# Optimization experiments

Measured on AMD Instinct MI355X. Metric: run time of the kernel, lower is better.

## Reference

```python
import jax, jax.numpy as jnp
import numpy as np

DIM_IN, DIM_Q, DIM_K, DIM_S, DIM_MLP_S, L, B = 512, 128, 128, 256, 128, 512, 32


def setup_inputs() -> dict:
    key = jax.random.key(0)
    ks = jax.random.split(key, 16)
    s = lambda fan_in: 1.0 / np.sqrt(fan_in)
    inp = {
        "query": jax.random.normal(ks[0], (B, L, DIM_IN), jnp.float32),
        "key": jax.random.normal(ks[1], (B, L, DIM_IN), jnp.float32),
        "value": jax.random.normal(ks[2], (B, L, DIM_IN), jnp.float32),
        "sf": jax.random.normal(ks[3], (B, DIM_S), jnp.float32),
        "atten_mask": jax.random.randint(ks[4], (B, L, L), 0, 2).astype(bool),
        # linear weights stored (in, out); y = x @ W + b
        "Wq": jax.random.normal(ks[5], (DIM_IN, DIM_Q), jnp.float32) * s(DIM_IN),
        "bq": jnp.zeros((DIM_Q,), jnp.float32),
        "Wk": jax.random.normal(ks[6], (DIM_IN, DIM_K), jnp.float32) * s(DIM_IN),
        "bk": jnp.zeros((DIM_K,), jnp.float32),
        "Wv": jax.random.normal(ks[7], (DIM_IN, DIM_K), jnp.float32) * s(DIM_IN),
        "bv": jnp.zeros((DIM_K,), jnp.float32),
        "Wb1": jax.random.normal(ks[8], (DIM_S, DIM_MLP_S), jnp.float32) * s(DIM_S),
        "bb1": jnp.zeros((DIM_MLP_S,), jnp.float32),
        "Wb2": jax.random.normal(ks[9], (DIM_MLP_S, L * L), jnp.float32) * s(DIM_MLP_S),
        "bb2": jnp.zeros((L * L,), jnp.float32),
    }
    return inp


def reference(query, key, value, sf, atten_mask, Wq, bq, Wk, bk, Wv, bv, Wb1, bb1, Wb2, bb2):
    b, l, d = query.shape
    q = query @ Wq + bq          # [b, l, dim_q]
    k = key @ Wk + bk            # [b, l, dim_k]
    v = value @ Wv + bv          # [b, l, dim_k]
    # bias MLP: Linear -> ReLU -> Linear, reshaped to [b, l, l]
    bias = (jax.nn.relu(sf @ Wb1 + bb1) @ Wb2 + bb2).reshape(b, l, l)
    scale = q.shape[-1] ** 0.5
    scores = jnp.einsum("bld,bmd->blm", q, k) / scale
    # faithful to masked_fill_(mask, 1e-9): masked positions become 1e-9, NOT -inf
    scores = jnp.where(atten_mask, jnp.asarray(1e-9, scores.dtype), scores)
    attn = jax.nn.softmax(scores, axis=-1) + bias   # bias added AFTER softmax
    out = jnp.einsum("blm,bmd->bld", attn, v)
    return out
```

## Files before the change

### kernel.cpp

```cpp
#include <hip/hip_runtime.h>


typedef unsigned int   u32;
typedef unsigned short u16;
typedef __attribute__((ext_vector_type(8))) short bf16x8;
typedef __attribute__((ext_vector_type(4))) float f32x4;
typedef __attribute__((ext_vector_type(4))) u32   u32x4;

__device__ __forceinline__ float B2F(u16 x) { return __uint_as_float(((u32)x) << 16); }
__device__ __forceinline__ u16 f2bf(float f) {
    u32 u = __float_as_uint(f);
    return (u16)((u + 0x7fffu + ((u >> 16) & 1u)) >> 16);
}

__global__ __launch_bounds__(256) void prep(
    const void* __restrict__ mask, u32* __restrict__ flag, int detN,
    const float* __restrict__ Wq, const float* __restrict__ Wk, const float* __restrict__ Wv,
    u16* __restrict__ WT,
    const float* __restrict__ sf, const float* __restrict__ Wb1,
    const float* __restrict__ bb1, float* __restrict__ hT)
{
    __shared__ u16 Ts[64][136];
    const int blk = blockIdx.x, tid = threadIdx.x;

    if (blk < detN) {
        const u32* m = (const u32*)mask;
        const size_t t = (size_t)blk * 256 + tid;
        u32 any = 0;
#pragma unroll
        for (int l = 0; l < 4; ++l) any |= (m[t * 4 + l] > 1u) ? 1u : 0u;
        if (__ballot(any)) {
            if ((tid & 63) == 0) atomicOr(flag, 1u);
        }
        return;
    }
    if (blk < detN + 24) {
        const int widx = blk - detN;
        const int s = widx >> 3, kt = widx & 7;
        const float* W = (s == 0) ? Wq : (s == 1) ? Wk : Wv;
        {
            const int kk = tid >> 2, nseg = tid & 3;
            const float4* src = (const float4*)(W + (size_t)(kt * 64 + kk) * 128 + nseg * 32);
#pragma unroll
            for (int j = 0; j < 8; ++j) {
                float4 v = src[j];
                Ts[kk][nseg * 32 + j * 4 + 0] = f2bf(v.x);
                Ts[kk][nseg * 32 + j * 4 + 1] = f2bf(v.y);
                Ts[kk][nseg * 32 + j * 4 + 2] = f2bf(v.z);
                Ts[kk][nseg * 32 + j * 4 + 3] = f2bf(v.w);
            }
        }
        __syncthreads();
        {
            const int n = tid >> 1, kseg = tid & 1;
            u32 pk[16];
#pragma unroll
            for (int j = 0; j < 16; ++j)
                pk[j] = (u32)Ts[kseg * 32 + 2 * j][n] | ((u32)Ts[kseg * 32 + 2 * j + 1][n] << 16);
            u32x4* dst = (u32x4*)(WT + (size_t)s * 65536 + (size_t)n * 512 + kt * 64 + kseg * 32);
            dst[0] = (u32x4){pk[0], pk[1], pk[2], pk[3]};
            dst[1] = (u32x4){pk[4], pk[5], pk[6], pk[7]};
            dst[2] = (u32x4){pk[8], pk[9], pk[10], pk[11]};
            dst[3] = (u32x4){pk[12], pk[13], pk[14], pk[15]};
        }
        return;
    }
    {
        const int t = (blk - detN - 24) * 256 + tid;
        const int b = t >> 7, n = t & 127;
        float acc = bb1[n];
        for (int m = 0; m < 256; ++m)
            acc += sf[b * 256 + m] * Wb1[m * 128 + n];
        hT[n * 32 + b] = fmaxf(acc, 0.0f);
    }
}

__global__ __launch_bounds__(256) void mid(
    const float* __restrict__ Xq, const float* __restrict__ Xk, const float* __restrict__ Xv,
    const u16* __restrict__ WT,
    const float* __restrict__ Bq, const float* __restrict__ Bk, const float* __restrict__ Bv,
    u16* __restrict__ Yq, u16* __restrict__ Yk, u16* __restrict__ YvT,
    const float* __restrict__ hT, const float* __restrict__ Wb2,
    const float* __restrict__ bb2, u16* __restrict__ biasb,
    const void* __restrict__ mask, const u32* __restrict__ flag, int mode,
    unsigned char* __restrict__ canonbuf)
{
    __shared__ u16 Xs[64][72];
    __shared__ u16 Ws[128][72];
    const int blk = blockIdx.x, tid = threadIdx.x;

    if (blk < 512) {
        const size_t n0 = ((size_t)blk * 256 + tid) * 2;
        float ax[32], ay[32];
        {
            const float2 bb = *(const float2*)&bb2[n0];
#pragma unroll
            for (int b = 0; b < 32; ++b) { ax[b] = bb.x; ay[b] = bb.y; }
        }
#pragma unroll 2
        for (int m = 0; m < 128; ++m) {
            const float2 w2 = *(const float2*)&Wb2[(size_t)m * 262144 + n0];
            const float* hrow = hT + m * 32;
#pragma unroll
            for (int b = 0; b < 32; ++b) {
                const float hv = hrow[b];
                ax[b] += w2.x * hv;
                ay[b] += w2.y * hv;
            }
        }
#pragma unroll
        for (int b = 0; b < 32; ++b) {
            const u32 pk = (u32)f2bf(ax[b]) | ((u32)f2bf(ay[b]) << 16);
            *(u32*)(biasb + (size_t)b * 262144 + n0) = pk;
        }
        return;
    }

    if (blk < 1280) {
        const int pidx = blk - 512;
        const int s = pidx >> 8;
        const int R0 = (pidx & 255) * 64;
        const float* X; const float* Bi;
        if (s == 0)      { X = Xq; Bi = Bq; }
        else if (s == 1) { X = Xk; Bi = Bk; }
        else             { X = Xv; Bi = Bv; }
        const u16* Wn = WT + (size_t)s * 65536;

        const int w    = tid >> 6;
        const int lane = tid & 63;
        const int c    = lane & 15;
        const int qd   = lane >> 4;

        f32x4 acc[8];
#pragma unroll
        for (int t = 0; t < 8; ++t) acc[t] = (f32x4){0.f, 0.f, 0.f, 0.f};

        for (int kc = 0; kc < 8; ++kc) {
            __syncthreads();
            {
                const int row = tid >> 2, seg = tid & 3;
                const float4* src = (const float4*)(X + (size_t)(R0 + row) * 512 + kc * 64 + seg * 16);
                float4 v0 = src[0], v1 = src[1], v2 = src[2], v3 = src[3];
                u32 pk[8];
                pk[0] = (u32)f2bf(v0.x) | ((u32)f2bf(v0.y) << 16);
                pk[1] = (u32)f2bf(v0.z) | ((u32)f2bf(v0.w) << 16);
                pk[2] = (u32)f2bf(v1.x) | ((u32)f2bf(v1.y) << 16);
                pk[3] = (u32)f2bf(v1.z) | ((u32)f2bf(v1.w) << 16);
                pk[4] = (u32)f2bf(v2.x) | ((u32)f2bf(v2.y) << 16);
                pk[5] = (u32)f2bf(v2.z) | ((u32)f2bf(v2.w) << 16);
                pk[6] = (u32)f2bf(v3.x) | ((u32)f2bf(v3.y) << 16);
                pk[7] = (u32)f2bf(v3.z) | ((u32)f2bf(v3.w) << 16);
                u32x4* dst = (u32x4*)&Xs[row][seg * 16];
                dst[0] = (u32x4){pk[0], pk[1], pk[2], pk[3]};
                dst[1] = (u32x4){pk[4], pk[5], pk[6], pk[7]};
            }
            {
                const int n = tid >> 1, seg = tid & 1;
                const u32x4* src = (const u32x4*)(Wn + (size_t)n * 512 + kc * 64 + seg * 32);
                u32x4 v0 = src[0], v1 = src[1], v2 = src[2], v3 = src[3];
                u32x4* dst = (u32x4*)&Ws[n][seg * 32];
                dst[0] = v0; dst[1] = v1; dst[2] = v2; dst[3] = v3;
            }
            __syncthreads();

#pragma unroll
            for (int ks = 0; ks < 2; ++ks) {
                if (s < 2) {
                    const bf16x8 a = *(const bf16x8*)&Xs[w * 16 + c][ks * 32 + qd * 8];
#pragma unroll
                    for (int nt = 0; nt < 8; ++nt) {
                        const bf16x8 b = *(const bf16x8*)&Ws[nt * 16 + c][ks * 32 + qd * 8];
                        acc[nt] = __builtin_amdgcn_mfma_f32_16x16x32_bf16(a, b, acc[nt], 0, 0, 0);
                    }
                } else {
#pragma unroll
                    for (int t = 0; t < 2; ++t) {
                        const bf16x8 a = *(const bf16x8*)&Ws[(2 * w + t) * 16 + c][ks * 32 + qd * 8];
#pragma unroll
                        for (int it = 0; it < 4; ++it) {
                            const bf16x8 b = *(const bf16x8*)&Xs[it * 16 + c][ks * 32 + qd * 8];
                            acc[t * 4 + it] = __builtin_amdgcn_mfma_f32_16x16x32_bf16(a, b, acc[t * 4 + it], 0, 0, 0);
                        }
                    }
                }
            }
        }

        if (s < 2) {
            u16* Y = (s == 0) ? Yq : Yk;
#pragma unroll
            for (int nt = 0; nt < 8; ++nt) {
                const float bn = Bi[nt * 16 + c];
#pragma unroll
                for (int r = 0; r < 4; ++r)
                    Y[(size_t)(R0 + w * 16 + qd * 4 + r) * 128 + nt * 16 + c] = f2bf(acc[nt][r] + bn);
            }
        } else {
            const int bb = (pidx & 255) >> 3, il0 = R0 & 511;
#pragma unroll
            for (int t = 0; t < 2; ++t)
#pragma unroll
                for (int r = 0; r < 4; ++r) {
                    const int d = (2 * w + t) * 16 + qd * 4 + r;
                    const float bd = Bi[d];
#pragma unroll
                    for (int it = 0; it < 4; ++it)
                        YvT[(size_t)bb * 65536 + (size_t)d * 512 + il0 + it * 16 + c] =
                            f2bf(acc[t * 4 + it][r] + bd);
                }
        }
        return;
    }

    {
        const int cb = blk - 1280;
        const size_t base = (size_t)cb * 4096;
        const bool i32src = (mode == 2) || (mode == 0 && *flag == 0);
        if (i32src) {
            const int* mi = (const int*)mask;
#pragma unroll
            for (int j = 0; j < 16; ++j) {
                const size_t i = base + (size_t)j * 256 + tid;
                canonbuf[i] = mi[i] ? 1 : 0;
            }
        } else {
            const unsigned char* mb = (const unsigned char*)mask;
#pragma unroll
            for (int j = 0; j < 16; ++j) {
                const size_t i = base + (size_t)j * 256 + tid;
                canonbuf[i] = mb[i] ? 1 : 0;
            }
        }
    }
}

__global__ __launch_bounds__(512, 2) void attn_mfma8(
    const u16* __restrict__ qb, const u16* __restrict__ kb, const u16* __restrict__ vTb,
    const unsigned char* __restrict__ canon, const u16* __restrict__ biasb,
    float* __restrict__ out)
{
    __shared__ alignas(16) u16 Ks[2][64 * 136];
    __shared__ alignas(16) u16 Ps[2][64 * 72];
    __shared__ alignas(16) u16 Vs[2][128 * 72];
    __shared__ alignas(16) u16 Bs[2][64 * 72];
    __shared__ float redm[2][64];
    __shared__ float reds[2][64];

    const int tid  = threadIdx.x;
    const int g    = tid >> 8;
    const int gtid = tid & 255;
    const int wl   = (tid >> 6) & 3;
    const int lane = tid & 63;
    const int c    = lane & 15;
    const int qd   = lane >> 4;
    const int bb   = blockIdx.x & 31;
    const int it   = blockIdx.x >> 5;
    const int i0   = it * 64;

    bf16x8 qf[4];
    {
        const u16* qp = qb + ((size_t)bb * 512 + i0 + wl * 16 + c) * 128 + qd * 8;
#pragma unroll
        for (int kc = 0; kc < 4; ++kc) qf[kc] = *(const bf16x8*)(qp + kc * 32);
    }

    const int kr_ = gtid >> 2, ksg = gtid & 3;
    const u16* kbase = kb + ((size_t)bb * 512 + g * 256) * 128;
    {
        const u32x4* src = (const u32x4*)(kbase + (size_t)kr_ * 128 + ksg * 32);
        u32x4 k0 = src[0], k1 = src[1], k2 = src[2], k3 = src[3];
        u32x4* dst = (u32x4*)&Ks[g][kr_ * 136 + ksg * 32];
        dst[0] = k0; dst[1] = k1; dst[2] = k2; dst[3] = k3;
    }
    __syncthreads();

    f32x4 S[4][4];
#pragma unroll
    for (int jt = 0; jt < 4; ++jt)
#pragma unroll
        for (int jj = 0; jj < 4; ++jj) S[jt][jj] = (f32x4){0.f, 0.f, 0.f, 0.f};

#pragma unroll
    for (int jt = 0; jt < 4; ++jt) {
        u32x4 k0, k1, k2, k3;
        if (jt < 3) {
            const u32x4* src = (const u32x4*)(kbase + ((size_t)(jt + 1) * 64 + kr_) * 128 + ksg * 32);
            k0 = src[0]; k1 = src[1]; k2 = src[2]; k3 = src[3];
        }
#pragma unroll
        for (int kc = 0; kc < 4; ++kc) {
            const bf16x8 a = qf[kc];
#pragma unroll
            for (int jj = 0; jj < 4; ++jj) {
                const bf16x8 b = *(const bf16x8*)&Ks[g][(jj * 16 + c) * 136 + kc * 32 + qd * 8];
                S[jt][jj] = __builtin_amdgcn_mfma_f32_16x16x32_bf16(a, b, S[jt][jj], 0, 0, 0);
            }
        }
        if (jt < 3) {
            __syncthreads();
            u32x4* dst = (u32x4*)&Ks[g][kr_ * 136 + ksg * 32];
            dst[0] = k0; dst[1] = k1; dst[2] = k2; dst[3] = k3;
            __syncthreads();
        }
    }

    const int vd = gtid >> 1, vsg = gtid & 1;
    const int brw = gtid >> 2, bsg = gtid & 3;
    const u16* vbase = vTb + (size_t)bb * 65536;
    const u16* bbase = biasb + (size_t)bb * 262144;
    u32x4 vr0, vr1, vr2, vr3, br0, br1;
    {
        const u32x4* sv = (const u32x4*)(vbase + (size_t)vd * 512 + (g * 4) * 64 + vsg * 32);
        vr0 = sv[0]; vr1 = sv[1]; vr2 = sv[2]; vr3 = sv[3];
        const u32x4* sb = (const u32x4*)(bbase + (size_t)(i0 + brw) * 512 + (g * 4) * 64 + bsg * 16);
        br0 = sb[0]; br1 = sb[1];
    }

    const float sc = 0.08838834764831845f;
    float lm[4];
#pragma unroll
    for (int r = 0; r < 4; ++r) {
        const int lrow = wl * 16 + qd * 4 + r;
        const unsigned char* cp = canon + ((size_t)bb * 512 + i0 + lrow) * 512 + g * 256;
        float mx = -3.4e38f;
#pragma unroll
        for (int jt = 0; jt < 4; ++jt)
#pragma unroll
            for (int jj = 0; jj < 4; ++jj) {
                float s = S[jt][jj][r] * sc;
                if (cp[jt * 64 + jj * 16 + c]) s = 1e-9f;
                S[jt][jj][r] = s;
                mx = fmaxf(mx, s);
            }
#pragma unroll
        for (int o = 1; o < 16; o <<= 1) mx = fmaxf(mx, __shfl_xor(mx, o, 64));
        lm[r] = mx;
    }
    if (c == 0) {
#pragma unroll
        for (int r = 0; r < 4; ++r) redm[g][wl * 16 + qd * 4 + r] = lm[r];
    }
    __syncthreads();
    float ls[4];
#pragma unroll
    for (int r = 0; r < 4; ++r) {
        const int lrow = wl * 16 + qd * 4 + r;
        const float gmx = fmaxf(redm[0][lrow], redm[1][lrow]);
        float sm = 0.f;
#pragma unroll
        for (int jt = 0; jt < 4; ++jt)
#pragma unroll
            for (int jj = 0; jj < 4; ++jj) {
                const float e = __expf(S[jt][jj][r] - gmx);
                S[jt][jj][r] = e;
                sm += e;
            }
#pragma unroll
        for (int o = 1; o < 16; o <<= 1) sm += __shfl_xor(sm, o, 64);
        ls[r] = sm;
    }
    if (c == 0) {
#pragma unroll
        for (int r = 0; r < 4; ++r) reds[g][wl * 16 + qd * 4 + r] = ls[r];
    }
    __syncthreads();
    float inv_[4];
#pragma unroll
    for (int r = 0; r < 4; ++r) {
        const int lrow = wl * 16 + qd * 4 + r;
        inv_[r] = 1.0f / (reds[0][lrow] + reds[1][lrow]);
    }

    f32x4 O_[8];
#pragma unroll
    for (int ns = 0; ns < 8; ++ns) O_[ns] = (f32x4){0.f, 0.f, 0.f, 0.f};

#pragma unroll
    for (int jt = 0; jt < 4; ++jt) {
        __syncthreads();
        {
            u32x4* dv = (u32x4*)&Vs[g][vd * 72 + vsg * 32];
            dv[0] = vr0; dv[1] = vr1; dv[2] = vr2; dv[3] = vr3;
            u32x4* db = (u32x4*)&Bs[g][brw * 72 + bsg * 16];
            db[0] = br0; db[1] = br1;
        }
        __syncthreads();
        if (jt < 3) {
            const int tg = g * 4 + jt + 1;
            const u32x4* sv = (const u32x4*)(vbase + (size_t)vd * 512 + tg * 64 + vsg * 32);
            vr0 = sv[0]; vr1 = sv[1]; vr2 = sv[2]; vr3 = sv[3];
            const u32x4* sb = (const u32x4*)(bbase + (size_t)(i0 + brw) * 512 + tg * 64 + bsg * 16);
            br0 = sb[0]; br1 = sb[1];
        }
#pragma unroll
        for (int r = 0; r < 4; ++r) {
            const int lrow = wl * 16 + qd * 4 + r;
#pragma unroll
            for (int jj = 0; jj < 4; ++jj) {
                const float p = S[jt][jj][r] * inv_[r] + B2F(Bs[g][lrow * 72 + jj * 16 + c]);
                Ps[g][lrow * 72 + jj * 16 + c] = f2bf(p);
            }
        }
        __syncthreads();
#pragma unroll
        for (int kc = 0; kc < 2; ++kc) {
            const bf16x8 a = *(const bf16x8*)&Ps[g][(wl * 16 + c) * 72 + kc * 32 + qd * 8];
#pragma unroll
            for (int ns = 0; ns < 8; ++ns) {
                const bf16x8 b = *(const bf16x8*)&Vs[g][(ns * 16 + c) * 72 + kc * 32 + qd * 8];
                O_[ns] = __builtin_amdgcn_mfma_f32_16x16x32_bf16(a, b, O_[ns], 0, 0, 0);
            }
        }
    }

    __syncthreads();
    float* Oc = (float*)&Ks[0][0];
    if (g == 1) {
#pragma unroll
        for (int ns = 0; ns < 8; ++ns)
#pragma unroll
            for (int r = 0; r < 4; ++r)
                Oc[(wl * 16 + qd * 4 + r) * 128 + ns * 16 + c] = O_[ns][r];
    }
    __syncthreads();
    if (g == 0) {
#pragma unroll
        for (int ns = 0; ns < 8; ++ns)
#pragma unroll
            for (int r = 0; r < 4; ++r)
                Oc[(wl * 16 + qd * 4 + r) * 128 + ns * 16 + c] += O_[ns][r];
    }
    __syncthreads();
    {
        const int row = tid >> 3, sg = tid & 7;
        const float4* s4 = (const float4*)&Oc[row * 128 + sg * 16];
        float4* d4 = (float4*)(out + ((size_t)bb * 512 + i0 + row) * 128 + sg * 16);
        d4[0] = s4[0]; d4[1] = s4[1]; d4[2] = s4[2]; d4[3] = s4[3];
    }
}

extern "C" void kernel_launch(void* const* d_in, const int* in_sizes, int n_in,
                              void* d_out, int out_size, void* d_ws, size_t ws_size,
                              hipStream_t stream)
{
    const float* query = (const float*)d_in[0];
    const float* key_  = (const float*)d_in[1];
    const float* value = (const float*)d_in[2];
    const float* sf    = (const float*)d_in[3];
    const void*  mask  = d_in[4];
    const float* Wq  = (const float*)d_in[5];
    const float* bq  = (const float*)d_in[6];
    const float* Wk  = (const float*)d_in[7];
    const float* bk  = (const float*)d_in[8];
    const float* Wv  = (const float*)d_in[9];
    const float* bv  = (const float*)d_in[10];
    const float* Wb1 = (const float*)d_in[11];
    const float* bb1 = (const float*)d_in[12];
    const float* Wb2 = (const float*)d_in[13];
    const float* bb2 = (const float*)d_in[14];
    float* out = (float*)d_out;

    char* w = (char*)d_ws;
    u32*   flag     = (u32*)(w);
    unsigned char* canonbuf = (unsigned char*)(w + (1u << 20));
    u16*   qb    = (u16*)(w + (16u << 20));
    u16*   kb    = (u16*)(w + (24u << 20));
    u16*   vTb   = (u16*)(w + (32u << 20));
    float* hT    = (float*)(w + (40u << 20));
    u16*   biasb = (u16*)(w + (41u << 20));
    u16*   WT    = (u16*)(w + (58u << 20));

    int mode = 0;
    if (n_in >= 15 && in_sizes[0] == 33554432) {
        if (in_sizes[4] == 8388608)       mode = 1;
        else if (in_sizes[4] == 33554432) mode = 2;
    }
    if (mode == 0) hipMemsetAsync(flag, 0, 4, stream);

    const int detN = (mode == 0) ? 2048 : 0;
    prep<<<detN + 40, 256, 0, stream>>>(mask, flag, detN, Wq, Wk, Wv, WT,
                                        sf, Wb1, bb1, hT);

    const int canN = (mode != 1) ? 2048 : 0;
    mid<<<1280 + canN, 256, 0, stream>>>(query, key_, value, WT,
                                         bq, bk, bv, qb, kb, vTb,
                                         hT, Wb2, bb2, biasb,
                                         mask, flag, mode, canonbuf);

    const unsigned char* canon = (mode == 1) ? (const unsigned char*)mask : canonbuf;
    attn_mfma8<<<256, 512, 0, stream>>>(qb, kb, vTb, canon, biasb, out);
}
```

Measured before the change: 345.2 us.

## Load projection A fragments directly from global, split bias MLP, vectorize mask canon

The QKV projection stops staging converted X tiles in LDS. Each wave now loads its fp32 fragments straight from global memory and converts them to bf16 in registers, which cuts LDS traffic and the matching writes. The bias MLP gets twice as many blocks, each thread computing one output column with a deeper unroll, to raise parallelism and reduce register pressure. Mask canonicalisation now uses 16-byte vector loads and stores with a SWAR byte test. The cost is redundant, less coalesced global reads of X across waves.

Result: slower. 363.4 us (+5.3%).

```diff
diff --git a/kernel.cpp b/kernel.cpp
--- a/kernel.cpp
+++ b/kernel.cpp
@@ -11,6 +11,18 @@
 __device__ __forceinline__ u16 f2bf(float f) {
     u32 u = __float_as_uint(f);
     return (u16)((u + 0x7fffu + ((u >> 16) & 1u)) >> 16);
+}
+
+__device__ __forceinline__ bf16x8 ldfragA(const float* __restrict__ p)
+{
+    const float4 v0 = *(const float4*)p;
+    const float4 v1 = *(const float4*)(p + 4);
+    union { u32 u[4]; bf16x8 h; } r;
+    r.u[0] = (u32)f2bf(v0.x) | ((u32)f2bf(v0.y) << 16);
+    r.u[1] = (u32)f2bf(v0.z) | ((u32)f2bf(v0.w) << 16);
+    r.u[2] = (u32)f2bf(v1.x) | ((u32)f2bf(v1.y) << 16);
+    r.u[3] = (u32)f2bf(v1.z) | ((u32)f2bf(v1.w) << 16);
+    return r.h;
 }
 
 __global__ __launch_bounds__(256) void prep(
@@ -85,39 +97,32 @@
     const void* __restrict__ mask, const u32* __restrict__ flag, int mode,
     unsigned char* __restrict__ canonbuf)
 {
-    __shared__ u16 Xs[64][72];
     __shared__ u16 Ws[128][72];
     const int blk = blockIdx.x, tid = threadIdx.x;
 
-    if (blk < 512) {
-        const size_t n0 = ((size_t)blk * 256 + tid) * 2;
-        float ax[32], ay[32];
+    if (blk < 1024) {
+        const size_t n = (size_t)blk * 256 + tid;
+        float acc[32];
         {
-            const float2 bb = *(const float2*)&bb2[n0];
-#pragma unroll
-            for (int b = 0; b < 32; ++b) { ax[b] = bb.x; ay[b] = bb.y; }
-        }
-#pragma unroll 2
+            const float bb = bb2[n];
+#pragma unroll
+            for (int b = 0; b < 32; ++b) acc[b] = bb;
+        }
+#pragma unroll 8
         for (int m = 0; m < 128; ++m) {
-            const float2 w2 = *(const float2*)&Wb2[(size_t)m * 262144 + n0];
+            const float wv = Wb2[(size_t)m * 262144 + n];
             const float* hrow = hT + m * 32;
 #pragma unroll
-            for (int b = 0; b < 32; ++b) {
-                const float hv = hrow[b];
-                ax[b] += w2.x * hv;
-                ay[b] += w2.y * hv;
-            }
-        }
-#pragma unroll
-        for (int b = 0; b < 32; ++b) {
-            const u32 pk = (u32)f2bf(ax[b]) | ((u32)f2bf(ay[b]) << 16);
-            *(u32*)(biasb + (size_t)b * 262144 + n0) = pk;
-        }
+            for (int b = 0; b < 32; ++b) acc[b] += wv * hrow[b];
+        }
+#pragma unroll
+        for (int b = 0; b < 32; ++b)
+            biasb[(size_t)b * 262144 + n] = f2bf(acc[b]);
         return;
     }
 
-    if (blk < 1280) {
-        const int pidx = blk - 512;
+    if (blk < 1792) {
+        const int pidx = blk - 1024;
         const int s = pidx >> 8;
         const int R0 = (pidx & 255) * 64;
         const float* X; const float* Bi;
@@ -138,23 +143,6 @@
         for (int kc = 0; kc < 8; ++kc) {
             __syncthreads();
             {
-                const int row = tid >> 2, seg = tid & 3;
-                const float4* src = (const float4*)(X + (size_t)(R0 + row) * 512 + kc * 64 + seg * 16);
-                float4 v0 = src[0], v1 = src[1], v2 = src[2], v3 = src[3];
-                u32 pk[8];
-                pk[0] = (u32)f2bf(v0.x) | ((u32)f2bf(v0.y) << 16);
-                pk[1] = (u32)f2bf(v0.z) | ((u32)f2bf(v0.w) << 16);
-                pk[2] = (u32)f2bf(v1.x) | ((u32)f2bf(v1.y) << 16);
-                pk[3] = (u32)f2bf(v1.z) | ((u32)f2bf(v1.w) << 16);
-                pk[4] = (u32)f2bf(v2.x) | ((u32)f2bf(v2.y) << 16);
-                pk[5] = (u32)f2bf(v2.z) | ((u32)f2bf(v2.w) << 16);
-                pk[6] = (u32)f2bf(v3.x) | ((u32)f2bf(v3.y) << 16);
-                pk[7] = (u32)f2bf(v3.z) | ((u32)f2bf(v3.w) << 16);
-                u32x4* dst = (u32x4*)&Xs[row][seg * 16];
-                dst[0] = (u32x4){pk[0], pk[1], pk[2], pk[3]};
-                dst[1] = (u32x4){pk[4], pk[5], pk[6], pk[7]};
-            }
-            {
                 const int n = tid >> 1, seg = tid & 1;
                 const u32x4* src = (const u32x4*)(Wn + (size_t)n * 512 + kc * 64 + seg * 32);
                 u32x4 v0 = src[0], v1 = src[1], v2 = src[2], v3 = src[3];
@@ -166,7 +154,8 @@
 #pragma unroll
             for (int ks = 0; ks < 2; ++ks) {
                 if (s < 2) {
-                    const bf16x8 a = *(const bf16x8*)&Xs[w * 16 + c][ks * 32 + qd * 8];
+                    const bf16x8 a = ldfragA(X + (size_t)(R0 + w * 16 + c) * 512
+                                               + kc * 64 + ks * 32 + qd * 8);
 #pragma unroll
                     for (int nt = 0; nt < 8; ++nt) {
                         const bf16x8 b = *(const bf16x8*)&Ws[nt * 16 + c][ks * 32 + qd * 8];
@@ -174,11 +163,12 @@
                     }
                 } else {
 #pragma unroll
-                    for (int t = 0; t < 2; ++t) {
-                        const bf16x8 a = *(const bf16x8*)&Ws[(2 * w + t) * 16 + c][ks * 32 + qd * 8];
-#pragma unroll
-                        for (int it = 0; it < 4; ++it) {
-                            const bf16x8 b = *(const bf16x8*)&Xs[it * 16 + c][ks * 32 + qd * 8];
+                    for (int it = 0; it < 4; ++it) {
+                        const bf16x8 b = ldfragA(X + (size_t)(R0 + it * 16 + c) * 512
+                                                   + kc * 64 + ks * 32 + qd * 8);
+#pragma unroll
+                        for (int t = 0; t < 2; ++t) {
+                            const bf16x8 a = *(const bf16x8*)&Ws[(2 * w + t) * 16 + c][ks * 32 + qd * 8];
                             acc[t * 4 + it] = __builtin_amdgcn_mfma_f32_16x16x32_bf16(a, b, acc[t * 4 + it], 0, 0, 0);
                         }
                     }
@@ -213,24 +203,27 @@
     }
 
     {
-        const int cb = blk - 1280;
-        const size_t base = (size_t)cb * 4096;
+        const int cb = blk - 1792;
+        const size_t base = (size_t)cb * 4096 + (size_t)tid * 16;
         const bool i32src = (mode == 2) || (mode == 0 && *flag == 0);
+        u32 wq[4];
         if (i32src) {
-            const int* mi = (const int*)mask;
-#pragma unroll
-            for (int j = 0; j < 16; ++j) {
-                const size_t i = base + (size_t)j * 256 + tid;
-                canonbuf[i] = mi[i] ? 1 : 0;
+            const int* mi = (const int*)mask + base;
+#pragma unroll
+            for (int q = 0; q < 4; ++q) {
+                const int4 v = *(const int4*)(mi + q * 4);
+                wq[q] = (v.x ? 1u : 0u) | ((v.y ? 1u : 0u) << 8)
+                      | ((v.z ? 1u : 0u) << 16) | ((v.w ? 1u : 0u) << 24);
             }
         } else {
-            const unsigned char* mb = (const unsigned char*)mask;
-#pragma unroll
-            for (int j = 0; j < 16; ++j) {
-                const size_t i = base + (size_t)j * 256 + tid;
-                canonbuf[i] = mb[i] ? 1 : 0;
-            }
-        }
+            const u32x4 v = *(const u32x4*)((const unsigned char*)mask + base);
+#pragma unroll
+            for (int q = 0; q < 4; ++q) {
+                const u32 x = v[q];
+                wq[q] = (((x & 0x7F7F7F7Fu) + 0x7F7F7F7Fu) | x) >> 7 & 0x01010101u;
+            }
+        }
+        *(u32x4*)(canonbuf + base) = (u32x4){wq[0], wq[1], wq[2], wq[3]};
     }
 }
 
@@ -482,7 +475,7 @@
                                         sf, Wb1, bb1, hT);
 
     const int canN = (mode != 1) ? 2048 : 0;
-    mid<<<1280 + canN, 256, 0, stream>>>(query, key_, value, WT,
+    mid<<<1792 + canN, 256, 0, stream>>>(query, key_, value, WT,
                                          bq, bk, bv, qb, kb, vTb,
                                          hT, Wb2, bb2, biasb,
                                          mask, flag, mode, canonbuf);
```
